# Performance work log

Measured on AMD Instinct MI355X. Metric: run time of the kernel, lower is better.

The kernel has to match this reference:

```python
import jax, jax.numpy as jnp
import numpy as np

KH, KW, PAD, G = 3, 3, 1, 4  # kernel, padding, deformable groups


def _bilinear_gather(xg, py, px):
    """xg: [B,G,C,Hin,Win]; py,px: [B,G,K,H,W] sample coords.
    Returns [B,G,C,K,H,W] with zero padding outside the image (mmcv semantics)."""
    B, Gd, C, Hin, Win = xg.shape
    y0 = jnp.floor(py)
    x0 = jnp.floor(px)
    wy1 = py - y0
    wx1 = px - x0
    wy0 = 1.0 - wy1
    wx0 = 1.0 - wx1
    xf = xg.reshape(B, Gd, C, Hin * Win)

    def gather(yi, xi):
        valid = (yi >= 0) & (yi < Hin) & (xi >= 0) & (xi < Win)
        yc = jnp.clip(yi, 0, Hin - 1).astype(jnp.int32)
        xc = jnp.clip(xi, 0, Win - 1).astype(jnp.int32)
        lin = (yc * Win + xc).reshape(B, Gd, 1, -1)  # [B,G,1,K*H*W]
        v = jnp.take_along_axis(xf, lin, axis=3).reshape(B, Gd, C, *yi.shape[2:])
        return v * valid[:, :, None].astype(xg.dtype)

    return (gather(y0, x0) * (wy0 * wx0)[:, :, None]
            + gather(y0, x0 + 1) * (wy0 * wx1)[:, :, None]
            + gather(y0 + 1, x0) * (wy1 * wx0)[:, :, None]
            + gather(y0 + 1, x0 + 1) * (wy1 * wx1)[:, :, None])


def setup_inputs() -> dict:
    key = jax.random.key(0)
    k1, k2, k3, k4 = jax.random.split(key, 4)
    B, Cin, Cout, H, W = 8, 256, 256, 64, 64
    x = jax.random.normal(k1, (B, Cin, H, W), dtype=jnp.float32)
    shape = jax.random.normal(k2, (B, 4, H, W), dtype=jnp.float32)
    # conv_offset: 1x1 conv, 4 -> G*2*KH*KW = 72 channels, no bias
    w_offset = jax.random.normal(k3, (G * 2 * KH * KW, 4), dtype=jnp.float32) * 0.1
    # conv_adaption: deform conv weight, no bias
    w_deform = jax.random.normal(k4, (Cout, Cin, KH, KW), dtype=jnp.float32) * 0.01
    return {"x": x, "shape": shape, "w_offset": w_offset, "w_deform": w_deform}


def reference(x, shape, w_offset, w_deform):
    B, Cin, H, W = x.shape
    Cout = w_deform.shape[0]
    K = KH * KW
    # 1x1 offset-predicting conv on detached shape
    shape = jax.lax.stop_gradient(shape)
    offset = jnp.einsum('oc,bchw->bohw', w_offset, shape)  # [B, G*2*K, H, W]
    off = offset.reshape(B, G, K, 2, H, W)  # mmcv layout: (dy, dx) per tap
    dy, dx = off[:, :, :, 0], off[:, :, :, 1]  # [B,G,K,H,W]
    # base sampling grid for each kernel tap
    ky, kx = jnp.meshgrid(jnp.arange(KH), jnp.arange(KW), indexing='ij')
    ky = ky.reshape(-1)
    kx = kx.reshape(-1)
    base_y = (ky - PAD)[:, None, None] + jnp.arange(H)[None, :, None]  # [K,H,1]
    base_x = (kx - PAD)[:, None, None] + jnp.arange(W)[None, None, :]  # [K,1,W]
    py = base_y[None, None].astype(x.dtype) + dy  # [B,G,K,H,W]
    px = base_x[None, None].astype(x.dtype) + dx
    xg = x.reshape(B, G, Cin // G, H, W)
    sampled = _bilinear_gather(xg, py, px)  # [B,G,Cpg,K,H,W]
    wr = w_deform.reshape(Cout, G, Cin // G, K)
    out = jnp.einsum('ogck,bgckhw->bohw', wr, sampled)
    return jax.nn.relu(out)
```

## Files before the change

### kernel.cpp

```cpp
#include <hip/hip_runtime.h>
#include <hip/hip_bf16.h>


#define Bn   8
#define CIN  256
#define COUT 256
#define Hn   64
#define Wn   64
#define Gn   4
#define Kn   9
#define CPG  64
#define GK   36

typedef __bf16 bf16x8 __attribute__((ext_vector_type(8)));
typedef float  f32x4  __attribute__((ext_vector_type(4)));
typedef _Float16 f16x2 __attribute__((ext_vector_type(2)));

#define SWPAD 1156
__global__ void fa_prep(const float* __restrict__ x, const float* __restrict__ w,
                        __bf16* __restrict__ xt, __bf16* __restrict__ wfrag) {
    const int bid = blockIdx.x, t = threadIdx.x;
    __shared__ __bf16 sw[16 * SWPAD];
    if (bid < 4096) {
        const int c8q = bid & 7, hwt = (bid >> 3) & 63, b = bid >> 9;
        const int hw = hwt * 64 + (t & 63);
        const int c8 = c8q * 4 + (t >> 6);
        const float* xp = x + ((size_t)(b * CIN + c8 * 8) << 12) + hw;
        bf16x8 v;
#pragma unroll
        for (int j = 0; j < 8; j++) v[j] = (__bf16)xp[(size_t)j << 12];
        *(bf16x8*)&xt[(((size_t)b << 12) + hw) * 256 + c8 * 8] = v;
    } else {
        const int mt = (bid - 4096) >> 1, gh = (bid - 4096) & 1;
        const int o0 = mt * 16, g0 = gh * 2;
        const int r = t >> 4, tr = t & 15;
        const float* wp = w + (size_t)(o0 + r) * (CIN * Kn) + g0 * (CPG * Kn);
#pragma unroll
        for (int it = 0; it < 18; it++) {
            int off = it * 64 + tr * 4;
            float4 v = *(const float4*)(wp + off);
            __bf16* d = &sw[r * SWPAD + off];
            d[0] = (__bf16)v.x; d[1] = (__bf16)v.y;
            d[2] = (__bf16)v.z; d[3] = (__bf16)v.w;
        }
        __syncthreads();
#pragma unroll
        for (int it = 0; it < 9; it++) {
            int chunk = it * 256 + t;
            int lane = chunk & 63, ks = (chunk >> 6) & 1, gkl = chunk >> 7;
            int gl = gkl / Kn, k = gkl - gl * Kn;
            int gk = g0 * Kn + gkl;
            int ol = lane & 15;
            int cbase = ks * 32 + (lane >> 4) * 8;
            bf16x8 v;
#pragma unroll
            for (int j = 0; j < 8; j++)
                v[j] = sw[ol * SWPAD + (gl * CPG + cbase + j) * Kn + k];
            *(bf16x8*)&wfrag[(((size_t)gk * 16 + mt) * 2 + ks) * 512 + lane * 8] = v;
        }
    }
}

__global__ __launch_bounds__(512, 4)
void fa_main(const __bf16* __restrict__ xt, const float* __restrict__ shp,
             const float* __restrict__ w_off, const __bf16* __restrict__ wfrag,
             float* __restrict__ out) {
    const int blk = blockIdx.x;
    const int bp = blk >> 7, h = (blk >> 1) & 63, wh = blk & 1;
    const int w0 = wh * 32;
    const int t = threadIdx.x;
    const int wid = t >> 6, lane = t & 63;
    const int col = lane & 15, quad = lane >> 4;
    const int cg = t & 7, nl = (t >> 3) & 63;

    __shared__ __align__(16) int4 s_meta[GK * 64];
    __shared__ __align__(16) __bf16 sB[2][64 * 64];
    __shared__ float s_shp[2 * 4 * 32];
    __shared__ float s_woff[GK * 8];

    if (t < 256) {
        int bb = t >> 7, c = (t >> 5) & 3, wl = t & 31;
        s_shp[t] = shp[(((bp * 2 + bb) * 4 + c) << 12) + h * Wn + w0 + wl];
    }
    for (int u = t; u < GK * 8; u += 512) s_woff[u] = w_off[u];
    __syncthreads();

    for (int i = t; i < GK * 64; i += 512) {
        int gk = i >> 6, n = i & 63;
        int bb = n >> 5, wl = n & 31;
        int g = gk / Kn, k = gk - g * Kn;
        int ky = k / 3, kx = k - ky * 3;
        float dy = 0.f, dx = 0.f;
#pragma unroll
        for (int c = 0; c < 4; c++) {
            float sv = s_shp[(bb * 4 + c) * 32 + wl];
            dy = fmaf(s_woff[gk * 8 + c],     sv, dy);
            dx = fmaf(s_woff[gk * 8 + 4 + c], sv, dx);
        }
        float py = (float)(h + ky - 1) + dy;
        float px = (float)(w0 + wl + kx - 1) + dx;
        float y0 = floorf(py), x0 = floorf(px);
        float fy = py - y0, fx = px - x0;
        int iy = (int)y0, ix = (int)x0;
        bool y0v = (unsigned)iy       < (unsigned)Hn;
        bool y1v = (unsigned)(iy + 1) < (unsigned)Hn;
        bool x0v = (unsigned)ix       < (unsigned)Wn;
        bool x1v = (unsigned)(ix + 1) < (unsigned)Wn;
        int yc0 = min(max(iy, 0), Hn - 1), yc1 = min(max(iy + 1, 0), Hn - 1);
        int xc0 = min(max(ix, 0), Wn - 1), xc1 = min(max(ix + 1, 0), Wn - 1);
        int l00 = yc0 * Wn + xc0, l01 = yc0 * Wn + xc1;
        int l10 = yc1 * Wn + xc0, l11 = yc1 * Wn + xc1;
        float wy1 = fy, wy0 = 1.f - fy, wx1 = fx, wx0 = 1.f - fx;
        float w00 = (y0v && x0v) ? wy0 * wx0 : 0.f;
        float w01 = (y0v && x1v) ? wy0 * wx1 : 0.f;
        float w10 = (y1v && x0v) ? wy1 * wx0 : 0.f;
        float w11 = (y1v && x1v) ? wy1 * wx1 : 0.f;
        f16x2 p0, p1;
        p0.x = (_Float16)w00; p0.y = (_Float16)w01;
        p1.x = (_Float16)w10; p1.y = (_Float16)w11;
        s_meta[i] = make_int4(l00 | (l01 << 16), l10 | (l11 << 16),
                              __builtin_bit_cast(int, p0),
                              __builtin_bit_cast(int, p1));
    }

    bf16x8 c4[4];
    int2   amv;

    auto issue = [&](int gk) {
        int4 mv = s_meta[gk * 64 + nl];
        amv.x = mv.z; amv.y = mv.w;
        int b = bp * 2 + (nl >> 5);
        int g = gk / Kn;
        const __bf16* base = xt + (((size_t)b << 12)) * 256 + g * CPG + cg * 8;
        c4[0] = *(const bf16x8*)(base + (size_t)(mv.x & 0xffff) * 256);
        c4[1] = *(const bf16x8*)(base + (size_t)((unsigned)mv.x >> 16) * 256);
        c4[2] = *(const bf16x8*)(base + (size_t)(mv.y & 0xffff) * 256);
        c4[3] = *(const bf16x8*)(base + (size_t)((unsigned)mv.y >> 16) * 256);
    };
    auto commit = [&](int buf) {
        f16x2 h0 = __builtin_bit_cast(f16x2, amv.x);
        f16x2 h1 = __builtin_bit_cast(f16x2, amv.y);
        float w00 = (float)h0.x, w01 = (float)h0.y;
        float w10 = (float)h1.x, w11 = (float)h1.y;
        bf16x8 r;
#pragma unroll
        for (int j = 0; j < 8; j++) {
            float v = w00 * (float)c4[0][j] + w01 * (float)c4[1][j]
                    + w10 * (float)c4[2][j] + w11 * (float)c4[3][j];
            r[j] = (__bf16)v;
        }
        *(bf16x8*)&sB[buf][(nl * 8 + (cg ^ (nl & 7))) * 8] = r;
    };

    f32x4 acc[2][4];
#pragma unroll
    for (int mt = 0; mt < 2; mt++)
#pragma unroll
        for (int nt = 0; nt < 4; nt++) acc[mt][nt] = (f32x4){0.f, 0.f, 0.f, 0.f};

    __syncthreads();

    issue(0);
    commit(0);
    issue(1);
    __syncthreads();

    for (int gk = 0; gk < GK; gk++) {
        const int buf = gk & 1;
        const __bf16* wbase = wfrag + (((size_t)gk * 16 + wid * 2) * 2) * 512;
        bf16x8 af[2][2];
#pragma unroll
        for (int ks = 0; ks < 2; ks++)
#pragma unroll
            for (int mt = 0; mt < 2; mt++)
                af[ks][mt] = *(const bf16x8*)(wbase + ((size_t)(mt * 2 + ks) * 64 + lane) * 8);
        if (gk + 1 < GK) commit(buf ^ 1);
        if (gk + 2 < GK) issue(gk + 2);
#pragma unroll
        for (int ks = 0; ks < 2; ks++) {
            bf16x8 bfv[4];
#pragma unroll
            for (int nt = 0; nt < 4; nt++) {
                int n = nt * 16 + col;
                int cq8 = ks * 4 + quad;
                bfv[nt] = *(const bf16x8*)&sB[buf][(n * 8 + (cq8 ^ (n & 7))) * 8];
            }
#pragma unroll
            for (int mt = 0; mt < 2; mt++)
#pragma unroll
                for (int nt = 0; nt < 4; nt++)
                    acc[mt][nt] = __builtin_amdgcn_mfma_f32_16x16x32_bf16(
                        af[ks][mt], bfv[nt], acc[mt][nt], 0, 0, 0);
        }
        __syncthreads();
    }

#pragma unroll
    for (int mt = 0; mt < 2; mt++)
#pragma unroll
        for (int r = 0; r < 4; r++) {
            int o = wid * 32 + mt * 16 + quad * 4 + r;
#pragma unroll
            for (int nt = 0; nt < 4; nt++) {
                int n = nt * 16 + col;
                int b = bp * 2 + (n >> 5);
                int w = w0 + (n & 31);
                out[(((size_t)(b * COUT + o)) << 12) + h * Wn + w] =
                    fmaxf(acc[mt][nt][r], 0.f);
            }
        }
}

extern "C" void kernel_launch(void* const* d_in, const int* in_sizes, int n_in,
                              void* d_out, int out_size, void* d_ws, size_t ws_size,
                              hipStream_t stream) {
    const float* x     = (const float*)d_in[0];
    const float* shp   = (const float*)d_in[1];
    const float* w_off = (const float*)d_in[2];
    const float* w_def = (const float*)d_in[3];
    float* out = (float*)d_out;
    __bf16* wfrag = (__bf16*)d_ws;
    __bf16* xt    = (__bf16*)((char*)d_ws + (2u << 20));

    fa_prep<<<4096 + 32, 256, 0, stream>>>(x, w_def, xt, wfrag);
    fa_main<<<512, 512, 0, stream>>>(xt, shp, w_off, wfrag, out);
}
```

Measured before the change: 146.4 us.

## Double N tile to full row with 1024-thread blocks and per-group metadata

Each block now covers a full 64-wide output row for two batches (N=128) with 16 waves, two along N and eight along M, so every weight fragment loaded from global memory is reused across twice as many columns. The sampling metadata shrinks to one deformable group at a time and is recomputed at group boundaries inside the main loop, with an extra barrier, which keeps LDS usage bounded. The grid halves to 256 blocks of 1024 threads, which cuts parallelism across CUs and adds sync stalls at each group switch.

```diff
diff --git a/kernel.cpp b/kernel.cpp
--- a/kernel.cpp
+++ b/kernel.cpp
@@ -61,76 +61,78 @@
     }
 }
 
-__global__ __launch_bounds__(512, 4)
+__global__ __launch_bounds__(1024, 4)
 void fa_main(const __bf16* __restrict__ xt, const float* __restrict__ shp,
              const float* __restrict__ w_off, const __bf16* __restrict__ wfrag,
              float* __restrict__ out) {
     const int blk = blockIdx.x;
-    const int bp = blk >> 7, h = (blk >> 1) & 63, wh = blk & 1;
-    const int w0 = wh * 32;
+    const int bp = blk >> 6, h = blk & 63;
     const int t = threadIdx.x;
     const int wid = t >> 6, lane = t & 63;
+    const int wid_m = wid & 7, wid_n = wid >> 3;
     const int col = lane & 15, quad = lane >> 4;
-    const int cg = t & 7, nl = (t >> 3) & 63;
-
-    __shared__ __align__(16) int4 s_meta[GK * 64];
-    __shared__ __align__(16) __bf16 sB[2][64 * 64];
-    __shared__ float s_shp[2 * 4 * 32];
+    const int cg = t & 7, nl = t >> 3;
+
+    __shared__ __align__(16) int4 s_meta[9 * 128];
+    __shared__ __align__(16) __bf16 sB[2][128 * 64];
+    __shared__ float s_shp[2 * 4 * 64];
     __shared__ float s_woff[GK * 8];
 
-    if (t < 256) {
-        int bb = t >> 7, c = (t >> 5) & 3, wl = t & 31;
-        s_shp[t] = shp[(((bp * 2 + bb) * 4 + c) << 12) + h * Wn + w0 + wl];
+    if (t < 512) {
+        int bb = t >> 8, c = (t >> 6) & 3, wl = t & 63;
+        s_shp[t] = shp[(((bp * 2 + bb) * 4 + c) << 12) + h * Wn + wl];
     }
-    for (int u = t; u < GK * 8; u += 512) s_woff[u] = w_off[u];
+    for (int u = t; u < GK * 8; u += 1024) s_woff[u] = w_off[u];
     __syncthreads();
 
-    for (int i = t; i < GK * 64; i += 512) {
-        int gk = i >> 6, n = i & 63;
-        int bb = n >> 5, wl = n & 31;
-        int g = gk / Kn, k = gk - g * Kn;
-        int ky = k / 3, kx = k - ky * 3;
-        float dy = 0.f, dx = 0.f;
-#pragma unroll
-        for (int c = 0; c < 4; c++) {
-            float sv = s_shp[(bb * 4 + c) * 32 + wl];
-            dy = fmaf(s_woff[gk * 8 + c],     sv, dy);
-            dx = fmaf(s_woff[gk * 8 + 4 + c], sv, dx);
-        }
-        float py = (float)(h + ky - 1) + dy;
-        float px = (float)(w0 + wl + kx - 1) + dx;
-        float y0 = floorf(py), x0 = floorf(px);
-        float fy = py - y0, fx = px - x0;
-        int iy = (int)y0, ix = (int)x0;
-        bool y0v = (unsigned)iy       < (unsigned)Hn;
-        bool y1v = (unsigned)(iy + 1) < (unsigned)Hn;
-        bool x0v = (unsigned)ix       < (unsigned)Wn;
-        bool x1v = (unsigned)(ix + 1) < (unsigned)Wn;
-        int yc0 = min(max(iy, 0), Hn - 1), yc1 = min(max(iy + 1, 0), Hn - 1);
-        int xc0 = min(max(ix, 0), Wn - 1), xc1 = min(max(ix + 1, 0), Wn - 1);
-        int l00 = yc0 * Wn + xc0, l01 = yc0 * Wn + xc1;
-        int l10 = yc1 * Wn + xc0, l11 = yc1 * Wn + xc1;
-        float wy1 = fy, wy0 = 1.f - fy, wx1 = fx, wx0 = 1.f - fx;
-        float w00 = (y0v && x0v) ? wy0 * wx0 : 0.f;
-        float w01 = (y0v && x1v) ? wy0 * wx1 : 0.f;
-        float w10 = (y1v && x0v) ? wy1 * wx0 : 0.f;
-        float w11 = (y1v && x1v) ? wy1 * wx1 : 0.f;
-        f16x2 p0, p1;
-        p0.x = (_Float16)w00; p0.y = (_Float16)w01;
-        p1.x = (_Float16)w10; p1.y = (_Float16)w11;
-        s_meta[i] = make_int4(l00 | (l01 << 16), l10 | (l11 << 16),
-                              __builtin_bit_cast(int, p0),
-                              __builtin_bit_cast(int, p1));
-    }
+    auto computeMeta = [&](int p) {
+        for (int i = t; i < 9 * 128; i += 1024) {
+            int gkl = i >> 7, n = i & 127;
+            int bb = n >> 6, wl = n & 63;
+            int gk = p * 9 + gkl;
+            int ky = gkl / 3, kx = gkl - ky * 3;
+            float dy = 0.f, dx = 0.f;
+#pragma unroll
+            for (int c = 0; c < 4; c++) {
+                float sv = s_shp[(bb * 4 + c) * 64 + wl];
+                dy = fmaf(s_woff[gk * 8 + c],     sv, dy);
+                dx = fmaf(s_woff[gk * 8 + 4 + c], sv, dx);
+            }
+            float py = (float)(h + ky - 1) + dy;
+            float px = (float)(wl + kx - 1) + dx;
+            float y0 = floorf(py), x0 = floorf(px);
+            float fy = py - y0, fx = px - x0;
+            int iy = (int)y0, ix = (int)x0;
+            bool y0v = (unsigned)iy       < (unsigned)Hn;
+            bool y1v = (unsigned)(iy + 1) < (unsigned)Hn;
+            bool x0v = (unsigned)ix       < (unsigned)Wn;
+            bool x1v = (unsigned)(ix + 1) < (unsigned)Wn;
+            int yc0 = min(max(iy, 0), Hn - 1), yc1 = min(max(iy + 1, 0), Hn - 1);
+            int xc0 = min(max(ix, 0), Wn - 1), xc1 = min(max(ix + 1, 0), Wn - 1);
+            int l00 = yc0 * Wn + xc0, l01 = yc0 * Wn + xc1;
+            int l10 = yc1 * Wn + xc0, l11 = yc1 * Wn + xc1;
+            float wy1 = fy, wy0 = 1.f - fy, wx1 = fx, wx0 = 1.f - fx;
+            float w00 = (y0v && x0v) ? wy0 * wx0 : 0.f;
+            float w01 = (y0v && x1v) ? wy0 * wx1 : 0.f;
+            float w10 = (y1v && x0v) ? wy1 * wx0 : 0.f;
+            float w11 = (y1v && x1v) ? wy1 * wx1 : 0.f;
+            f16x2 p0, p1;
+            p0.x = (_Float16)w00; p0.y = (_Float16)w01;
+            p1.x = (_Float16)w10; p1.y = (_Float16)w11;
+            s_meta[i] = make_int4(l00 | (l01 << 16), l10 | (l11 << 16),
+                                  __builtin_bit_cast(int, p0),
+                                  __builtin_bit_cast(int, p1));
+        }
+    };
 
     bf16x8 c4[4];
     int2   amv;
 
     auto issue = [&](int gk) {
-        int4 mv = s_meta[gk * 64 + nl];
+        int g = gk / 9;
+        int4 mv = s_meta[(gk - g * 9) * 128 + nl];
         amv.x = mv.z; amv.y = mv.w;
-        int b = bp * 2 + (nl >> 5);
-        int g = gk / Kn;
+        int b = bp * 2 + (nl >> 6);
         const __bf16* base = xt + (((size_t)b << 12)) * 256 + g * CPG + cg * 8;
         c4[0] = *(const bf16x8*)(base + (size_t)(mv.x & 0xffff) * 256);
         c4[1] = *(const bf16x8*)(base + (size_t)((unsigned)mv.x >> 16) * 256);
@@ -158,6 +160,7 @@
 #pragma unroll
         for (int nt = 0; nt < 4; nt++) acc[mt][nt] = (f32x4){0.f, 0.f, 0.f, 0.f};
 
+    computeMeta(0);
     __syncthreads();
 
     issue(0);
@@ -167,7 +170,7 @@
 
     for (int gk = 0; gk < GK; gk++) {
         const int buf = gk & 1;
-        const __bf16* wbase = wfrag + (((size_t)gk * 16 + wid * 2) * 2) * 512;
+        const __bf16* wbase = wfrag + (((size_t)gk * 16 + wid_m * 2) * 2) * 512;
         bf16x8 af[2][2];
 #pragma unroll
         for (int ks = 0; ks < 2; ks++)
@@ -175,13 +178,17 @@
             for (int mt = 0; mt < 2; mt++)
                 af[ks][mt] = *(const bf16x8*)(wbase + ((size_t)(mt * 2 + ks) * 64 + lane) * 8);
         if (gk + 1 < GK) commit(buf ^ 1);
+        if (gk == 7 || gk == 16 || gk == 25) {
+            computeMeta((gk + 2) / 9);
+            __syncthreads();
+        }
         if (gk + 2 < GK) issue(gk + 2);
 #pragma unroll
         for (int ks = 0; ks < 2; ks++) {
             bf16x8 bfv[4];
 #pragma unroll
             for (int nt = 0; nt < 4; nt++) {
-                int n = nt * 16 + col;
+                int n = wid_n * 64 + nt * 16 + col;
                 int cq8 = ks * 4 + quad;
                 bfv[nt] = *(const bf16x8*)&sB[buf][(n * 8 + (cq8 ^ (n & 7))) * 8];
             }
@@ -195,16 +202,15 @@
         __syncthreads();
     }
 
+    const int b = bp * 2 + wid_n;
 #pragma unroll
     for (int mt = 0; mt < 2; mt++)
 #pragma unroll
         for (int r = 0; r < 4; r++) {
-            int o = wid * 32 + mt * 16 + quad * 4 + r;
+            int o = wid_m * 32 + mt * 16 + quad * 4 + r;
 #pragma unroll
             for (int nt = 0; nt < 4; nt++) {
-                int n = nt * 16 + col;
-                int b = bp * 2 + (n >> 5);
-                int w = w0 + (n & 31);
+                int w = nt * 16 + col;
                 out[(((size_t)(b * COUT + o)) << 12) + h * Wn + w] =
                     fmaxf(acc[mt][nt][r], 0.f);
             }
@@ -223,5 +229,5 @@
     __bf16* xt    = (__bf16*)((char*)d_ws + (2u << 20));
 
     fa_prep<<<4096 + 32, 256, 0, stream>>>(x, w_def, xt, wfrag);
-    fa_main<<<512, 512, 0, stream>>>(xt, shp, w_off, wfrag, out);
+    fa_main<<<256, 1024, 0, stream>>>(xt, shp, w_off, wfrag, out);
 }
```

After: 151.7 us. 3.7% more time.

## Switch to fp16 operands with packed bilinear math and 32x32x16 MFMA tiles

Applied to the files above, without the earlier changes.

Changes the intermediate transposed input and weight fragments from bf16 to fp16. The bilinear interpolation then runs as packed fp16 multiply-adds instead of per-element fp32 math with conversions. The GEMM moves from 16x16x32 bf16 MFMA to 32x32x16 fp16 MFMA, with the weight fragment layout rebuilt and the output write pattern changed to match. The aim is fewer VALU instructions in the commit stage and fewer, larger MFMAs, at the cost of fp16 range limits and reduced accumulation precision in the interpolation.

```diff
diff --git a/kernel.cpp b/kernel.cpp
--- a/kernel.cpp
+++ b/kernel.cpp
@@ -12,69 +12,74 @@
 #define CPG  64
 #define GK   36
 
-typedef __bf16 bf16x8 __attribute__((ext_vector_type(8)));
-typedef float  f32x4  __attribute__((ext_vector_type(4)));
+typedef _Float16 f16x8 __attribute__((ext_vector_type(8)));
 typedef _Float16 f16x2 __attribute__((ext_vector_type(2)));
-
-#define SWPAD 1156
+typedef float    f32x16 __attribute__((ext_vector_type(16)));
+
+static __device__ __forceinline__ f16x2 pair_of(const f16x8& v, int r) {
+    int4 u = __builtin_bit_cast(int4, v);
+    int  p = (r == 0) ? u.x : (r == 1) ? u.y : (r == 2) ? u.z : u.w;
+    return __builtin_bit_cast(f16x2, p);
+}
+
+#define SWPAD 578
 __global__ void fa_prep(const float* __restrict__ x, const float* __restrict__ w,
-                        __bf16* __restrict__ xt, __bf16* __restrict__ wfrag) {
+                        _Float16* __restrict__ xt, _Float16* __restrict__ wfrag) {
     const int bid = blockIdx.x, t = threadIdx.x;
-    __shared__ __bf16 sw[16 * SWPAD];
+    __shared__ _Float16 sw[32 * SWPAD];
     if (bid < 4096) {
         const int c8q = bid & 7, hwt = (bid >> 3) & 63, b = bid >> 9;
         const int hw = hwt * 64 + (t & 63);
         const int c8 = c8q * 4 + (t >> 6);
         const float* xp = x + ((size_t)(b * CIN + c8 * 8) << 12) + hw;
-        bf16x8 v;
-#pragma unroll
-        for (int j = 0; j < 8; j++) v[j] = (__bf16)xp[(size_t)j << 12];
-        *(bf16x8*)&xt[(((size_t)b << 12) + hw) * 256 + c8 * 8] = v;
+        f16x8 v;
+#pragma unroll
+        for (int j = 0; j < 8; j++) v[j] = (_Float16)xp[(size_t)j << 12];
+        *(f16x8*)&xt[(((size_t)b << 12) + hw) * 256 + c8 * 8] = v;
     } else {
-        const int mt = (bid - 4096) >> 1, gh = (bid - 4096) & 1;
-        const int o0 = mt * 16, g0 = gh * 2;
-        const int r = t >> 4, tr = t & 15;
-        const float* wp = w + (size_t)(o0 + r) * (CIN * Kn) + g0 * (CPG * Kn);
+        const int bid2 = bid - 4096;
+        const int mt8 = bid2 >> 2, g = bid2 & 3;
+        const int r = t >> 3, tr = t & 7;
+        const float* wp = w + (size_t)(mt8 * 32 + r) * (CIN * Kn) + g * (CPG * Kn);
 #pragma unroll
         for (int it = 0; it < 18; it++) {
-            int off = it * 64 + tr * 4;
+            int off = it * 32 + tr * 4;
             float4 v = *(const float4*)(wp + off);
-            __bf16* d = &sw[r * SWPAD + off];
-            d[0] = (__bf16)v.x; d[1] = (__bf16)v.y;
-            d[2] = (__bf16)v.z; d[3] = (__bf16)v.w;
+            _Float16* d = &sw[r * SWPAD + off];
+            d[0] = (_Float16)v.x; d[1] = (_Float16)v.y;
+            d[2] = (_Float16)v.z; d[3] = (_Float16)v.w;
         }
         __syncthreads();
 #pragma unroll
         for (int it = 0; it < 9; it++) {
             int chunk = it * 256 + t;
-            int lane = chunk & 63, ks = (chunk >> 6) & 1, gkl = chunk >> 7;
-            int gl = gkl / Kn, k = gkl - gl * Kn;
-            int gk = g0 * Kn + gkl;
-            int ol = lane & 15;
-            int cbase = ks * 32 + (lane >> 4) * 8;
-            bf16x8 v;
+            int lane = chunk & 63, ks4 = (chunk >> 6) & 3, k9 = chunk >> 8;
+            int gk = g * Kn + k9;
+            int ol = lane & 31;
+            int cbase = ks4 * 16 + (lane >> 5) * 8;
+            f16x8 v;
 #pragma unroll
             for (int j = 0; j < 8; j++)
-                v[j] = sw[ol * SWPAD + (gl * CPG + cbase + j) * Kn + k];
-            *(bf16x8*)&wfrag[(((size_t)gk * 16 + mt) * 2 + ks) * 512 + lane * 8] = v;
+                v[j] = sw[ol * SWPAD + (cbase + j) * Kn + k9];
+            *(f16x8*)&wfrag[(((size_t)gk * 8 + mt8) * 4 + ks4) * 512 + lane * 8] = v;
         }
     }
 }
 
 __global__ __launch_bounds__(512, 4)
-void fa_main(const __bf16* __restrict__ xt, const float* __restrict__ shp,
-             const float* __restrict__ w_off, const __bf16* __restrict__ wfrag,
+void fa_main(const _Float16* __restrict__ xt, const float* __restrict__ shp,
+             const float* __restrict__ w_off, const _Float16* __restrict__ wfrag,
              float* __restrict__ out) {
     const int blk = blockIdx.x;
     const int bp = blk >> 7, h = (blk >> 1) & 63, wh = blk & 1;
     const int w0 = wh * 32;
     const int t = threadIdx.x;
     const int wid = t >> 6, lane = t & 63;
-    const int col = lane & 15, quad = lane >> 4;
+    const int l31 = lane & 31, lhi = lane >> 5;
     const int cg = t & 7, nl = (t >> 3) & 63;
 
     __shared__ __align__(16) int4 s_meta[GK * 64];
-    __shared__ __align__(16) __bf16 sB[2][64 * 64];
+    __shared__ __align__(16) _Float16 sB[2][64 * 64];
     __shared__ float s_shp[2 * 4 * 32];
     __shared__ float s_woff[GK * 8];
 
@@ -123,40 +128,46 @@
                               __builtin_bit_cast(int, p1));
     }
 
-    bf16x8 c4[4];
-    int2   amv;
+    f16x8 c4[4];
+    int2  amv;
 
     auto issue = [&](int gk) {
         int4 mv = s_meta[gk * 64 + nl];
         amv.x = mv.z; amv.y = mv.w;
         int b = bp * 2 + (nl >> 5);
         int g = gk / Kn;
-        const __bf16* base = xt + (((size_t)b << 12)) * 256 + g * CPG + cg * 8;
-        c4[0] = *(const bf16x8*)(base + (size_t)(mv.x & 0xffff) * 256);
-        c4[1] = *(const bf16x8*)(base + (size_t)((unsigned)mv.x >> 16) * 256);
-        c4[2] = *(const bf16x8*)(base + (size_t)(mv.y & 0xffff) * 256);
-        c4[3] = *(const bf16x8*)(base + (size_t)((unsigned)mv.y >> 16) * 256);
+        const _Float16* base = xt + (((size_t)b << 12)) * 256 + g * CPG + cg * 8;
+        c4[0] = *(const f16x8*)(base + (size_t)(mv.x & 0xffff) * 256);
+        c4[1] = *(const f16x8*)(base + (size_t)((unsigned)mv.x >> 16) * 256);
+        c4[2] = *(const f16x8*)(base + (size_t)(mv.y & 0xffff) * 256);
+        c4[3] = *(const f16x8*)(base + (size_t)((unsigned)mv.y >> 16) * 256);
     };
     auto commit = [&](int buf) {
         f16x2 h0 = __builtin_bit_cast(f16x2, amv.x);
         f16x2 h1 = __builtin_bit_cast(f16x2, amv.y);
-        float w00 = (float)h0.x, w01 = (float)h0.y;
-        float w10 = (float)h1.x, w11 = (float)h1.y;
-        bf16x8 r;
-#pragma unroll
-        for (int j = 0; j < 8; j++) {
-            float v = w00 * (float)c4[0][j] + w01 * (float)c4[1][j]
-                    + w10 * (float)c4[2][j] + w11 * (float)c4[3][j];
-            r[j] = (__bf16)v;
-        }
-        *(bf16x8*)&sB[buf][(nl * 8 + (cg ^ (nl & 7))) * 8] = r;
+        f16x2 a00; a00.x = h0.x; a00.y = h0.x;
+        f16x2 a01; a01.x = h0.y; a01.y = h0.y;
+        f16x2 a10; a10.x = h1.x; a10.y = h1.x;
+        f16x2 a11; a11.x = h1.y; a11.y = h1.y;
+        int4 rp;
+#pragma unroll
+        for (int r = 0; r < 4; r++) {
+            f16x2 s = a00 * pair_of(c4[0], r);
+            s = a01 * pair_of(c4[1], r) + s;
+            s = a10 * pair_of(c4[2], r) + s;
+            s = a11 * pair_of(c4[3], r) + s;
+            int sv = __builtin_bit_cast(int, s);
+            if (r == 0) rp.x = sv; else if (r == 1) rp.y = sv;
+            else if (r == 2) rp.z = sv; else rp.w = sv;
+        }
+        *(int4*)&sB[buf][(nl * 8 + (cg ^ (nl & 7))) * 8] = rp;
     };
 
-    f32x4 acc[2][4];
-#pragma unroll
-    for (int mt = 0; mt < 2; mt++)
-#pragma unroll
-        for (int nt = 0; nt < 4; nt++) acc[mt][nt] = (f32x4){0.f, 0.f, 0.f, 0.f};
+    f32x16 acc[2];
+#pragma unroll
+    for (int nt = 0; nt < 2; nt++)
+#pragma unroll
+        for (int r = 0; r < 16; r++) acc[nt][r] = 0.f;
 
     __syncthreads();
 
@@ -167,48 +178,38 @@
 
     for (int gk = 0; gk < GK; gk++) {
         const int buf = gk & 1;
-        const __bf16* wbase = wfrag + (((size_t)gk * 16 + wid * 2) * 2) * 512;
-        bf16x8 af[2][2];
-#pragma unroll
-        for (int ks = 0; ks < 2; ks++)
-#pragma unroll
-            for (int mt = 0; mt < 2; mt++)
-                af[ks][mt] = *(const bf16x8*)(wbase + ((size_t)(mt * 2 + ks) * 64 + lane) * 8);
+        const _Float16* wbase = wfrag + (((size_t)gk * 8 + wid) * 4) * 512;
+        f16x8 af[4];
+#pragma unroll
+        for (int ks = 0; ks < 4; ks++)
+            af[ks] = *(const f16x8*)(wbase + ((size_t)ks * 64 + lane) * 8);
         if (gk + 1 < GK) commit(buf ^ 1);
         if (gk + 2 < GK) issue(gk + 2);
 #pragma unroll
-        for (int ks = 0; ks < 2; ks++) {
-            bf16x8 bfv[4];
-#pragma unroll
-            for (int nt = 0; nt < 4; nt++) {
-                int n = nt * 16 + col;
-                int cq8 = ks * 4 + quad;
-                bfv[nt] = *(const bf16x8*)&sB[buf][(n * 8 + (cq8 ^ (n & 7))) * 8];
+        for (int ks = 0; ks < 4; ks++) {
+            int cb = ks * 2 + lhi;
+#pragma unroll
+            for (int nt = 0; nt < 2; nt++) {
+                int n = nt * 32 + l31;
+                f16x8 bf = *(const f16x8*)&sB[buf][(n * 8 + (cb ^ (n & 7))) * 8];
+                acc[nt] = __builtin_amdgcn_mfma_f32_32x32x16_f16(
+                    af[ks], bf, acc[nt], 0, 0, 0);
             }
-#pragma unroll
-            for (int mt = 0; mt < 2; mt++)
-#pragma unroll
-                for (int nt = 0; nt < 4; nt++)
-                    acc[mt][nt] = __builtin_amdgcn_mfma_f32_16x16x32_bf16(
-                        af[ks][mt], bfv[nt], acc[mt][nt], 0, 0, 0);
         }
         __syncthreads();
     }
 
 #pragma unroll
-    for (int mt = 0; mt < 2; mt++)
-#pragma unroll
-        for (int r = 0; r < 4; r++) {
-            int o = wid * 32 + mt * 16 + quad * 4 + r;
-#pragma unroll
-            for (int nt = 0; nt < 4; nt++) {
-                int n = nt * 16 + col;
-                int b = bp * 2 + (n >> 5);
-                int w = w0 + (n & 31);
-                out[(((size_t)(b * COUT + o)) << 12) + h * Wn + w] =
-                    fmaxf(acc[mt][nt][r], 0.f);
-            }
-        }
+    for (int nt = 0; nt < 2; nt++) {
+        int b = bp * 2 + nt;
+        float* op = out + ((size_t)b * COUT << 12) + h * Wn + w0 + l31;
+#pragma unroll
+        for (int reg = 0; reg < 16; reg++) {
+            int row = (reg & 3) + 8 * (reg >> 2) + 4 * lhi;
+            int o = wid * 32 + row;
+            op[(size_t)o << 12] = fmaxf(acc[nt][reg], 0.f);
+        }
+    }
 }
 
 extern "C" void kernel_launch(void* const* d_in, const int* in_sizes, int n_in,
@@ -219,8 +220,8 @@
     const float* w_off = (const float*)d_in[2];
     const float* w_def = (const float*)d_in[3];
     float* out = (float*)d_out;
-    __bf16* wfrag = (__bf16*)d_ws;
-    __bf16* xt    = (__bf16*)((char*)d_ws + (2u << 20));
+    _Float16* wfrag = (_Float16*)d_ws;
+    _Float16* xt    = (_Float16*)((char*)d_ws + (2u << 20));
 
     fa_prep<<<4096 + 32, 256, 0, stream>>>(x, w_def, xt, wfrag);
     fa_main<<<512, 512, 0, stream>>>(xt, shp, w_off, wfrag, out);
```

Measured after the change: 147.7 us. About the same (+0.9%).
